# Performance work log

Hardware: AMD Instinct MI355X
Metric: run time of the kernel (lower is better)

The kernel has to match this reference:

```python
import jax, jax.numpy as jnp
import numpy as np

B, IN_F, K_INT, OUT_F = 256, 512, 75, 64
INIT = 0.05


def setup_inputs() -> dict:
    key = jax.random.key(0)
    k_x, k_t = jax.random.split(key)
    x = jax.random.normal(k_x, (B, IN_F), dtype=jnp.float32)
    T = jax.random.normal(k_t, (IN_F, K_INT, OUT_F), dtype=jnp.float32) * INIT
    return {"x": x, "T": T}


def reference(x, T):
    # M: [B, K, O] = x @ T flattened over (K, O)
    Bn = x.shape[0]
    M = (x @ T.reshape(T.shape[0], -1)).reshape(Bn, T.shape[1], T.shape[2])
    # pairwise L1 distance over K: [B, B, O]
    # (original materializes [B, B, K, O] broadcasted diff; same math)
    M_diff = M[None, :, :, :] - M[:, None, :, :]
    distance = jnp.abs(M_diff).sum(axis=2)           # [B, B, O]
    exp_distance = jnp.exp(-distance)                # [B, B, O]
    minibatch_features = exp_distance.sum(axis=1) - 1.0  # [B, O]; -1 removes self-distance
    return minibatch_features
```

## Files before the change

### kernel.cpp

```cpp
#include <hip/hip_runtime.h>


typedef __attribute__((ext_vector_type(8))) short bf16x8;
typedef __attribute__((ext_vector_type(4))) float f32x4;
typedef unsigned short u16;
typedef unsigned int u32;

__device__ inline u16 f2bf(float f) {
  u32 u = __float_as_uint(f);
  return (u16)((u + 0x7FFFu + ((u >> 16) & 1u)) >> 16);
}

__global__ __launch_bounds__(256) void cvt_all(const float* __restrict__ x,
                                               const float* __restrict__ T,
                                               u16* __restrict__ xb,
                                               u16* __restrict__ Tb) {
  const int bid = blockIdx.x;
  const int tid = threadIdx.x;

  if (bid >= 600) {
    const int i = (bid - 600) * 256 + tid;
    const float4* x4 = reinterpret_cast<const float4*>(x);
    const float4 v0 = x4[i * 2], v1 = x4[i * 2 + 1];
    uint4 o;
    o.x = (u32)f2bf(v0.x) | ((u32)f2bf(v0.y) << 16);
    o.y = (u32)f2bf(v0.z) | ((u32)f2bf(v0.w) << 16);
    o.z = (u32)f2bf(v1.x) | ((u32)f2bf(v1.y) << 16);
    o.w = (u32)f2bf(v1.z) | ((u32)f2bf(v1.w) << 16);
    *reinterpret_cast<uint4*>(xb + i * 8) = o;
    return;
  }

  const int f0 = (bid & 7) << 6;
  const int k = bid >> 3;
  __shared__ float tile[64][65];

  const float4* T4 = reinterpret_cast<const float4*>(T);
  const int r = tid >> 2;
  const int c = tid & 3;
#pragma unroll
  for (int h = 0; h < 4; ++h) {
    const int q = c + (h << 2);
    const float4 v = T4[(f0 + r) * 1200 + k * 16 + q];
    tile[r][(q << 2) + 0] = v.x;
    tile[r][(q << 2) + 1] = v.y;
    tile[r][(q << 2) + 2] = v.z;
    tile[r][(q << 2) + 3] = v.w;
  }
  __syncthreads();

  const int w = tid >> 2;
  u16 us[16];
#pragma unroll
  for (int j = 0; j < 16; ++j) us[j] = f2bf(tile[(c << 4) + j][w]);
  uint4 p0, p1;
  p0.x = (u32)us[0] | ((u32)us[1] << 16);
  p0.y = (u32)us[2] | ((u32)us[3] << 16);
  p0.z = (u32)us[4] | ((u32)us[5] << 16);
  p0.w = (u32)us[6] | ((u32)us[7] << 16);
  p1.x = (u32)us[8] | ((u32)us[9] << 16);
  p1.y = (u32)us[10] | ((u32)us[11] << 16);
  p1.z = (u32)us[12] | ((u32)us[13] << 16);
  p1.w = (u32)us[14] | ((u32)us[15] << 16);
  uint4* dst = reinterpret_cast<uint4*>(Tb + ((k << 6) + w) * 512 + f0 + (c << 4));
  dst[0] = p0;
  dst[1] = p1;
}

__global__ __launch_bounds__(256) void md_gemm_mfma(const u16* __restrict__ Tb,
                                                    const u16* __restrict__ xb,
                                                    float* __restrict__ Mt) {
  const int tid = threadIdx.x;
  const int l = tid & 63, w = tid >> 6;
  const int n0 = (blockIdx.x << 6) + ((w >> 1) << 5);
  const int b0 = (blockIdx.y << 6) + ((w & 1) << 5);
  const int lr = l & 15;
  const int ko = (l >> 4) << 3;

  const u16* pa0 = Tb + (n0 + lr) * 512 + ko;
  const u16* pa1 = pa0 + 16 * 512;
  const u16* pb0 = xb + (b0 + lr) * 512 + ko;
  const u16* pb1 = pb0 + 16 * 512;

  f32x4 d00 = {0.f, 0.f, 0.f, 0.f}, d01 = d00, d10 = d00, d11 = d00;

#pragma unroll 4
  for (int kk = 0; kk < 16; ++kk) {
    const int off = kk << 5;
    const bf16x8 a0 = *reinterpret_cast<const bf16x8*>(pa0 + off);
    const bf16x8 a1 = *reinterpret_cast<const bf16x8*>(pa1 + off);
    const bf16x8 f0 = *reinterpret_cast<const bf16x8*>(pb0 + off);
    const bf16x8 f1 = *reinterpret_cast<const bf16x8*>(pb1 + off);
    d00 = __builtin_amdgcn_mfma_f32_16x16x32_bf16(a0, f0, d00, 0, 0, 0);
    d01 = __builtin_amdgcn_mfma_f32_16x16x32_bf16(a0, f1, d01, 0, 0, 0);
    d10 = __builtin_amdgcn_mfma_f32_16x16x32_bf16(a1, f0, d10, 0, 0, 0);
    d11 = __builtin_amdgcn_mfma_f32_16x16x32_bf16(a1, f1, d11, 0, 0, 0);
  }

#pragma unroll
  for (int r = 0; r < 4; ++r) {
    const int row = ((l >> 4) << 2) + r;
    {
      const int n = n0 + row;
      float* base = Mt + (n & 63) * 19200 + (n >> 6) * 256;
      base[b0 + lr] = d00[r];
      base[b0 + 16 + lr] = d01[r];
    }
    {
      const int n = n0 + 16 + row;
      float* base = Mt + (n & 63) * 19200 + (n >> 6) * 256;
      base[b0 + lr] = d10[r];
      base[b0 + 16 + lr] = d11[r];
    }
  }
}

__global__ __launch_bounds__(256, 1) void md_pair2(const float* __restrict__ Mt,
                                                   float* __restrict__ out) {
  const int bid = blockIdx.x;
  const int o = bid & 63;
  const int ibase = (bid >> 6) << 6;
  const int tid = threadIdx.x;

  __shared__ alignas(16) float Ms[75 * 256];

  {
    const float4* src = reinterpret_cast<const float4*>(Mt + o * 19200);
    float4* dst = reinterpret_cast<float4*>(Ms);
    for (int t = tid; t < 4800; t += 256) dst[t] = src[t];
  }
  __syncthreads();

  const int is = tid & 7;
  const int js = tid >> 3;
  const int ifq = ((ibase >> 2) + (is << 1));

  float d[8][8];
#pragma unroll
  for (int a = 0; a < 8; ++a)
#pragma unroll
    for (int b = 0; b < 8; ++b) d[a][b] = 0.0f;

#pragma unroll 2
  for (int k = 0; k < 75; ++k) {
    const float4* row4 = reinterpret_cast<const float4*>(Ms + (k << 8));
    const float4 vi0 = row4[ifq];
    const float4 vi1 = row4[ifq + 1];
    const float4 vj0 = row4[(js << 1)];
    const float4 vj1 = row4[(js << 1) + 1];
    const float ia[8] = {vi0.x, vi0.y, vi0.z, vi0.w, vi1.x, vi1.y, vi1.z, vi1.w};
    const float ja[8] = {vj0.x, vj0.y, vj0.z, vj0.w, vj1.x, vj1.y, vj1.z, vj1.w};
#pragma unroll
    for (int a = 0; a < 8; ++a)
#pragma unroll
      for (int b = 0; b < 8; ++b) d[a][b] += __builtin_fabsf(ja[b] - ia[a]);
  }

  float isum[8];
#pragma unroll
  for (int a = 0; a < 8; ++a) {
    float s = 0.0f;
#pragma unroll
    for (int b = 0; b < 8; ++b) s += __expf(-d[a][b]);
    isum[a] = s;
  }

#pragma unroll
  for (int m = 8; m <= 32; m <<= 1)
#pragma unroll
    for (int a = 0; a < 8; ++a) isum[a] += __shfl_xor(isum[a], m);

  __syncthreads();
  float* red = Ms;
  const int wv = tid >> 6;
  if (((tid >> 3) & 7) == 0) {
#pragma unroll
    for (int a = 0; a < 8; ++a) red[wv * 72 + (is << 3) + a] = isum[a];
  }
  __syncthreads();
  if (tid < 64) {
    const float s = red[tid] + red[72 + tid] + red[144 + tid] + red[216 + tid];
    out[(ibase + tid) * 64 + o] = s - 1.0f;
  }
}

extern "C" void kernel_launch(void* const* d_in, const int* in_sizes, int n_in,
                              void* d_out, int out_size, void* d_ws, size_t ws_size,
                              hipStream_t stream) {
  const float* x = (const float*)d_in[0];
  const float* T = (const float*)d_in[1];
  float* out = (float*)d_out;

  char* ws = (char*)d_ws;
  float* Mt = (float*)ws;
  u16* Tb = (u16*)(ws + 4915200);
  u16* xb = (u16*)(ws + 9830400);

  cvt_all<<<664, 256, 0, stream>>>(x, T, xb, Tb);
  md_gemm_mfma<<<dim3(75, 4), 256, 0, stream>>>(Tb, xb, Mt);
  md_pair2<<<256, 256, 0, stream>>>(Mt, out);
}
```

Measured before the change: 58.39 us.

## Split GEMM over K into two partials and shrink pairwise blocks with bf16 smem

The GEMM gets a z-dimension that splits the 512-long reduction into two halves, each writing its own partial M buffer, which doubles the number of GEMM blocks. The pairwise kernel now sums the two partials as it loads, stores the j-side values in LDS as bf16 and the i-side as fp32 in two K chunks, and uses 32 i-rows per block to launch 512 blocks without the one-block-per-CU launch bound. The diagonal is masked out explicitly instead of subtracting 1. The aim is more parallelism and lower LDS use per block for better occupancy, at the cost of extra partial-sum traffic and bf16 rounding of the j operand in the L1 distance.

```diff
diff --git a/kernel.cpp b/kernel.cpp
--- a/kernel.cpp
+++ b/kernel.cpp
@@ -10,6 +10,8 @@
   u32 u = __float_as_uint(f);
   return (u16)((u + 0x7FFFu + ((u >> 16) & 1u)) >> 16);
 }
+__device__ inline float bflo(u32 u) { return __uint_as_float(u << 16); }
+__device__ inline float bfhi(u32 u) { return __uint_as_float(u & 0xFFFF0000u); }
 
 __global__ __launch_bounds__(256) void cvt_all(const float* __restrict__ x,
                                                const float* __restrict__ T,
@@ -69,23 +71,24 @@
 
 __global__ __launch_bounds__(256) void md_gemm_mfma(const u16* __restrict__ Tb,
                                                     const u16* __restrict__ xb,
-                                                    float* __restrict__ Mt) {
+                                                    float* __restrict__ Mt2) {
   const int tid = threadIdx.x;
   const int l = tid & 63, w = tid >> 6;
   const int n0 = (blockIdx.x << 6) + ((w >> 1) << 5);
   const int b0 = (blockIdx.y << 6) + ((w & 1) << 5);
+  const int z = blockIdx.z;
   const int lr = l & 15;
   const int ko = (l >> 4) << 3;
 
-  const u16* pa0 = Tb + (n0 + lr) * 512 + ko;
+  const u16* pa0 = Tb + (n0 + lr) * 512 + z * 256 + ko;
   const u16* pa1 = pa0 + 16 * 512;
-  const u16* pb0 = xb + (b0 + lr) * 512 + ko;
+  const u16* pb0 = xb + (b0 + lr) * 512 + z * 256 + ko;
   const u16* pb1 = pb0 + 16 * 512;
 
   f32x4 d00 = {0.f, 0.f, 0.f, 0.f}, d01 = d00, d10 = d00, d11 = d00;
 
 #pragma unroll 4
-  for (int kk = 0; kk < 16; ++kk) {
+  for (int kk = 0; kk < 8; ++kk) {
     const int off = kk << 5;
     const bf16x8 a0 = *reinterpret_cast<const bf16x8*>(pa0 + off);
     const bf16x8 a1 = *reinterpret_cast<const bf16x8*>(pa1 + off);
@@ -97,6 +100,7 @@
     d11 = __builtin_amdgcn_mfma_f32_16x16x32_bf16(a1, f1, d11, 0, 0, 0);
   }
 
+  float* Mt = Mt2 + z * 1228800;
 #pragma unroll
   for (int r = 0; r < 4; ++r) {
     const int row = ((l >> 4) << 2) + r;
@@ -115,72 +119,86 @@
   }
 }
 
-__global__ __launch_bounds__(256, 1) void md_pair2(const float* __restrict__ Mt,
-                                                   float* __restrict__ out) {
+__global__ __launch_bounds__(256) void md_pair3(const float* __restrict__ Mt2,
+                                                float* __restrict__ out) {
   const int bid = blockIdx.x;
   const int o = bid & 63;
-  const int ibase = (bid >> 6) << 6;
+  const int it = bid >> 6;
+  const int ibase = it << 5;
   const int tid = threadIdx.x;
-
-  __shared__ alignas(16) float Ms[75 * 256];
-
-  {
-    const float4* src = reinterpret_cast<const float4*>(Mt + o * 19200);
-    float4* dst = reinterpret_cast<float4*>(Ms);
-    for (int t = tid; t < 4800; t += 256) dst[t] = src[t];
-  }
+  const int is = tid & 7;
+  const int jg = tid >> 3;
+
+  __shared__ alignas(16) u16 MjB[38 * 256];
+  __shared__ alignas(16) float MiF[38 * 32];
+
+  const float* M0 = Mt2 + o * 19200;
+  const float* M1 = M0 + 1228800;
+
+  float d[4][8];
+#pragma unroll
+  for (int a = 0; a < 4; ++a)
+#pragma unroll
+    for (int b = 0; b < 8; ++b) d[a][b] = 0.0f;
+
+  for (int h = 0; h < 2; ++h) {
+    const int kbase = h * 38;
+    const int nk = h ? 37 : 38;
+    __syncthreads();
+    for (int idx = tid; idx < nk * 64; idx += 256) {
+      const int kk = idx >> 6, q = idx & 63;
+      const int goff = (kbase + kk) * 256 + (q << 2);
+      const float4 v0 = *reinterpret_cast<const float4*>(M0 + goff);
+      const float4 v1 = *reinterpret_cast<const float4*>(M1 + goff);
+      uint2 p;
+      p.x = (u32)f2bf(v0.x + v1.x) | ((u32)f2bf(v0.y + v1.y) << 16);
+      p.y = (u32)f2bf(v0.z + v1.z) | ((u32)f2bf(v0.w + v1.w) << 16);
+      *reinterpret_cast<uint2*>(MjB + kk * 256 + (q << 2)) = p;
+    }
+    for (int idx = tid; idx < nk * 32; idx += 256) {
+      const int kk = idx >> 5, ii = idx & 31;
+      const int goff = (kbase + kk) * 256 + ibase + ii;
+      MiF[kk * 32 + ii] = M0[goff] + M1[goff];
+    }
+    __syncthreads();
+
+    for (int kk = 0; kk < nk; ++kk) {
+      const float4 vi = *reinterpret_cast<const float4*>(MiF + kk * 32 + (is << 2));
+      const uint4 ju = *reinterpret_cast<const uint4*>(MjB + kk * 256 + (jg << 3));
+      const float ia[4] = {vi.x, vi.y, vi.z, vi.w};
+      const float ja[8] = {bflo(ju.x), bfhi(ju.x), bflo(ju.y), bfhi(ju.y),
+                           bflo(ju.z), bfhi(ju.z), bflo(ju.w), bfhi(ju.w)};
+#pragma unroll
+      for (int a = 0; a < 4; ++a)
+#pragma unroll
+        for (int b = 0; b < 8; ++b) d[a][b] += __builtin_fabsf(ja[b] - ia[a]);
+    }
+  }
+
+  float s[4];
+#pragma unroll
+  for (int a = 0; a < 4; ++a) {
+    const int ia = ibase + (is << 2) + a;
+    float t = 0.0f;
+#pragma unroll
+    for (int b = 0; b < 8; ++b) {
+      const int j = (jg << 3) + b;
+      const float e = __expf(-d[a][b]);
+      t += (j == ia) ? 0.0f : e;
+    }
+    s[a] = t;
+  }
+
   __syncthreads();
-
-  const int is = tid & 7;
-  const int js = tid >> 3;
-  const int ifq = ((ibase >> 2) + (is << 1));
-
-  float d[8][8];
-#pragma unroll
-  for (int a = 0; a < 8; ++a)
-#pragma unroll
-    for (int b = 0; b < 8; ++b) d[a][b] = 0.0f;
-
-#pragma unroll 2
-  for (int k = 0; k < 75; ++k) {
-    const float4* row4 = reinterpret_cast<const float4*>(Ms + (k << 8));
-    const float4 vi0 = row4[ifq];
-    const float4 vi1 = row4[ifq + 1];
-    const float4 vj0 = row4[(js << 1)];
-    const float4 vj1 = row4[(js << 1) + 1];
-    const float ia[8] = {vi0.x, vi0.y, vi0.z, vi0.w, vi1.x, vi1.y, vi1.z, vi1.w};
-    const float ja[8] = {vj0.x, vj0.y, vj0.z, vj0.w, vj1.x, vj1.y, vj1.z, vj1.w};
-#pragma unroll
-    for (int a = 0; a < 8; ++a)
-#pragma unroll
-      for (int b = 0; b < 8; ++b) d[a][b] += __builtin_fabsf(ja[b] - ia[a]);
-  }
-
-  float isum[8];
-#pragma unroll
-  for (int a = 0; a < 8; ++a) {
-    float s = 0.0f;
-#pragma unroll
-    for (int b = 0; b < 8; ++b) s += __expf(-d[a][b]);
-    isum[a] = s;
-  }
-
-#pragma unroll
-  for (int m = 8; m <= 32; m <<= 1)
-#pragma unroll
-    for (int a = 0; a < 8; ++a) isum[a] += __shfl_xor(isum[a], m);
-
+  float* red = reinterpret_cast<float*>(MjB);
+#pragma unroll
+  for (int a = 0; a < 4; ++a) red[((is << 2) + a) * 33 + jg] = s[a];
   __syncthreads();
-  float* red = Ms;
-  const int wv = tid >> 6;
-  if (((tid >> 3) & 7) == 0) {
-#pragma unroll
-    for (int a = 0; a < 8; ++a) red[wv * 72 + (is << 3) + a] = isum[a];
-  }
-  __syncthreads();
-  if (tid < 64) {
-    const float s = red[tid] + red[72 + tid] + red[144 + tid] + red[216 + tid];
-    out[(ibase + tid) * 64 + o] = s - 1.0f;
+  if (tid < 32) {
+    float t = 0.0f;
+#pragma unroll
+    for (int g = 0; g < 32; ++g) t += red[tid * 33 + g];
+    out[(ibase + tid) * 64 + o] = t;
   }
 }
 
@@ -192,11 +210,11 @@
   float* out = (float*)d_out;
 
   char* ws = (char*)d_ws;
-  float* Mt = (float*)ws;
-  u16* Tb = (u16*)(ws + 4915200);
-  u16* xb = (u16*)(ws + 9830400);
+  float* Mt2 = (float*)ws;
+  u16* Tb = (u16*)(ws + 9830400);
+  u16* xb = (u16*)(ws + 14745600);
 
   cvt_all<<<664, 256, 0, stream>>>(x, T, xb, Tb);
-  md_gemm_mfma<<<dim3(75, 4), 256, 0, stream>>>(Tb, xb, Mt);
-  md_pair2<<<256, 256, 0, stream>>>(Mt, out);
-}
+  md_gemm_mfma<<<dim3(75, 4, 2), 256, 0, stream>>>(Tb, xb, Mt2);
+  md_pair3<<<512, 256, 0, stream>>>(Mt2, out);
+}
```

Measured after the change: 56.01 us. -4.1%, faster.
